# Optimization experiments

Measured on AMD Instinct MI355X. Metric: run time of the kernel, lower is better.

## Reference

```python
import jax, jax.numpy as jnp
import numpy as np

B, DIM, H, W = 4, 192, 256, 256
HEADS, DS = 6, 2
CPH = DIM // HEADS  # channels per head = 32
DN = ('NCHW', 'OIHW', 'NCHW')


def _conv(x, w, padding, groups=1):
    return jax.lax.conv_general_dilated(x, w, (1, 1), padding,
                                        dimension_numbers=DN,
                                        feature_group_count=groups)


def setup_inputs() -> dict:
    key = jax.random.key(0)
    ks = jax.random.split(key, 5)
    x = jax.random.normal(ks[0], (B, DIM, H, W), dtype=jnp.float32)
    temperature = jnp.ones((HEADS, 1, 1), dtype=jnp.float32)
    qkv_w = jax.random.normal(ks[1], (3 * DIM, DIM, 1, 1), dtype=jnp.float32) * 0.02
    dw_w = jax.random.normal(ks[2], (3 * DIM, 1, 3, 3), dtype=jnp.float32) * 0.02
    proj_w = jax.random.normal(ks[3], (DIM, DIM, 1, 1), dtype=jnp.float32) * 0.02
    a = jnp.full((1,), 0.2, dtype=jnp.float32)
    return {"x": x, "temperature": temperature, "qkv_w": qkv_w, "dw_w": dw_w,
            "proj_w": proj_w, "a1": a, "a2": a, "a3": a, "a4": a}


def _masked_softmax(attn, kk):
    # top-k mask per row (exact torch.topk + scatter_ semantics)
    _, idx = jax.lax.top_k(attn, kk)                      # [b,h,C,kk]
    mask = jax.nn.one_hot(idx, attn.shape[-1], dtype=jnp.bool_).any(axis=-2)
    return jax.nn.softmax(jnp.where(mask, attn, -jnp.inf), axis=-1)


def reference(x, temperature, qkv_w, dw_w, proj_w, a1, a2, a3, a4):
    b, c, h, w = x.shape
    h2, w2 = h // DS, w // DS
    # 1x1 qkv conv at full res, then exact adaptive (regular) max pool by DS
    qkv = _conv(x, qkv_w, 'VALID')                        # [b, 3*dim, h, w]
    qkv = jax.lax.reduce_window(qkv, -jnp.inf, jax.lax.max,
                                (1, 1, DS, DS), (1, 1, DS, DS), 'VALID')
    # depthwise 3x3
    qkv = _conv(qkv, dw_w, 'SAME', groups=3 * DIM)        # [b, 3*dim, h2, w2]
    q, k, v = jnp.split(qkv, 3, axis=1)
    n = h2 * w2
    q = q.reshape(b, HEADS, CPH, n)
    k = k.reshape(b, HEADS, CPH, n)
    v = v.reshape(b, HEADS, CPH, n)
    # F.normalize along last dim (eps clamp 1e-12)
    q = q / jnp.maximum(jnp.linalg.norm(q, axis=-1, keepdims=True), 1e-12)
    k = k / jnp.maximum(jnp.linalg.norm(k, axis=-1, keepdims=True), 1e-12)
    attn = jnp.einsum('bhcn,bhdn->bhcd', q, k) * temperature[None]  # [b,h,C,C]
    Cc = attn.shape[-1]
    att1 = _masked_softmax(attn, Cc // 2)
    att2 = _masked_softmax(attn, Cc * 2 // 3)
    att3 = _masked_softmax(attn, Cc * 3 // 4)
    att4 = _masked_softmax(attn, Cc * 4 // 5)
    def apply(a):
        return jnp.einsum('bhcd,bhdn->bhcn', a, v)
    out = apply(att1) * a1 + apply(att2) * a2 + apply(att3) * a3 + apply(att4) * a4
    out = out.reshape(b, DIM, h2, w2)
    out = jax.nn.gelu(out, approximate=False)
    # nearest upsample by integer factor DS
    out = jnp.repeat(jnp.repeat(out, DS, axis=2), DS, axis=3)
    out = _conv(out, proj_w, 'VALID')
    return out
```

## Files before the change

kernel.cpp:

```cpp
#include <hip/hip_runtime.h>
#include <hip/hip_bf16.h>
#include <math.h>

typedef __attribute__((ext_vector_type(8))) short bf16x8;
typedef __attribute__((ext_vector_type(4))) float f32x4;
typedef __attribute__((ext_vector_type(4))) unsigned int u32x4;

#define NP 16384
#define HWFULL 65536

__device__ __forceinline__ unsigned short f2bf(float f){
    union { float f; unsigned int u; } v; v.f = f;
    unsigned int u = v.u;
    u += 0x7fffu + ((u >> 16) & 1u);
    return (unsigned short)(u >> 16);
}
__device__ __forceinline__ float bf2f(unsigned short h){
    union { unsigned int u; float f; } v; v.u = ((unsigned int)h) << 16;
    return v.f;
}
__device__ __forceinline__ unsigned int pk2(float a, float b){
    return (unsigned int)f2bf(a) | ((unsigned int)f2bf(b) << 16);
}

__global__ void k_convert(const float* __restrict__ s, unsigned short* __restrict__ d, int n){
    int i = blockIdx.x * 256 + threadIdx.x;
    if (i < n) d[i] = f2bf(s[i]);
}

__global__ __launch_bounds__(256, 2)
void k_qkvpool(const float* __restrict__ x, const unsigned short* __restrict__ Wbf,
               unsigned short* __restrict__ qkvp){
    __shared__ unsigned short Bl[128*200];
    __shared__ unsigned short Ep[192*36];
    int tid = threadIdx.x;
    int lane = tid & 63, wv = tid >> 6;
    int n16 = lane & 15, quad = lane >> 4;
    int bx = blockIdx.x;
    int y2 = bx >> 2, x2blk = bx & 3;
    int b = blockIdx.y;

    #pragma unroll 6
    for (int j=0;j<12;j++){
        int idx = tid + j*256;
        int g = idx >> 7, w = idx & 127;
        int y = y2*2 + (w >> 6);
        int xc = x2blk*64 + (w & 63);
        const float* xp = x + (size_t)(b*192 + g*8) * HWFULL + y*256 + xc;
        float v0 = xp[0];
        float v1 = xp[(size_t)1*HWFULL];
        float v2 = xp[(size_t)2*HWFULL];
        float v3 = xp[(size_t)3*HWFULL];
        float v4 = xp[(size_t)4*HWFULL];
        float v5 = xp[(size_t)5*HWFULL];
        float v6 = xp[(size_t)6*HWFULL];
        float v7 = xp[(size_t)7*HWFULL];
        u32x4 pk;
        pk.x = pk2(v0,v1); pk.y = pk2(v2,v3); pk.z = pk2(v4,v5); pk.w = pk2(v6,v7);
        *(u32x4*)&Bl[w*200 + g*8] = pk;
    }
    bf16x8 afc[3], afn[3];
    #pragma unroll
    for (int j=0;j<3;j++)
        afc[j] = *(const bf16x8*)(Wbf + (size_t)(((wv*3+j)*16 + n16)*192 + quad*8));
    __syncthreads();

    for (int ocblk=0; ocblk<3; ocblk++){
        f32x4 acc[3][8];
        #pragma unroll
        for (int j=0;j<3;j++)
          #pragma unroll
          for (int s=0;s<8;s++)
            acc[j][s] = (f32x4){0.f,0.f,0.f,0.f};

        #pragma unroll 1
        for (int it=0; it<6; it++){
            int nocb = (it==5) ? ocblk+1 : ocblk;
            int nit  = (it==5) ? 0 : it+1;
            if (nocb < 3){
                #pragma unroll
                for (int j=0;j<3;j++)
                    afn[j] = *(const bf16x8*)(Wbf +
                        (size_t)((nocb*192 + (wv*3+j)*16 + n16)*192 + nit*32 + quad*8));
            }
            int bko = it*32 + quad*8;
            bf16x8 bfr[8];
            #pragma unroll
            for (int s=0;s<8;s++) bfr[s] = *(const bf16x8*)&Bl[(s*16 + n16)*200 + bko];
            #pragma unroll
            for (int j=0;j<3;j++)
              #pragma unroll
              for (int s=0;s<8;s++)
                acc[j][s] = __builtin_amdgcn_mfma_f32_16x16x32_bf16(afc[j], bfr[s], acc[j][s], 0,0,0);
            #pragma unroll
            for (int j=0;j<3;j++) afc[j] = afn[j];
        }
        __syncthreads();
        #pragma unroll
        for (int j=0;j<3;j++){
            int ocr = (wv*3+j)*16 + quad*4;
            #pragma unroll
            for (int sp=0;sp<4;sp++){
                #pragma unroll
                for (int r=0;r<4;r++){
                    float v = fmaxf(acc[j][sp][r], acc[j][sp+4][r]);
                    float o = __shfl_xor(v, 1, 64);
                    v = fmaxf(v, o);
                    if ((n16 & 1) == 0)
                        Ep[(ocr + r)*36 + sp*8 + (n16 >> 1)] = f2bf(v);
                }
            }
        }
        __syncthreads();
        size_t rowbase = (size_t)(b*576 + ocblk*192)*NP + y2*128 + x2blk*32;
        #pragma unroll
        for (int it=0; it<6; it++){
            int c = tid + it*256;
            int row = c >> 3, seg = c & 7;
            uint2 vv = *(const uint2*)&Ep[row*36 + seg*4];
            *(uint2*)(qkvp + rowbase + (size_t)row*NP + seg*4) = vv;
        }
    }
}

__global__ void k_dwconv(const unsigned short* __restrict__ qkvp, const float* __restrict__ dww,
                         float* __restrict__ dwout, float* __restrict__ sumsq){
    __shared__ float sl[18*130];
    int tid = threadIdx.x;
    int y0 = blockIdx.x * 16;
    int ch = blockIdx.y;
    int b  = blockIdx.z;
    const unsigned short* in = qkvp + (size_t)(b*576 + ch) * NP;
    #pragma unroll
    for (int j=0;j<10;j++){
        int idx = tid + j*256;
        if (idx < 18*130){
            int row = idx / 130;
            int col = idx % 130;
            int gy = y0 - 1 + row;
            int gx = col - 1;
            float v = 0.f;
            if (gy >= 0 && gy < 128 && gx >= 0 && gx < 128)
                v = bf2f(in[gy*128 + gx]);
            sl[idx] = v;
        }
    }
    float w0 = dww[ch*9+0], w1 = dww[ch*9+1], w2 = dww[ch*9+2];
    float w3 = dww[ch*9+3], w4 = dww[ch*9+4], w5 = dww[ch*9+5];
    float w6 = dww[ch*9+6], w7 = dww[ch*9+7], w8 = dww[ch*9+8];
    __syncthreads();
    float* outp = dwout + (size_t)(b*576 + ch) * NP;
    int col = tid & 127, half = tid >> 7;
    float ssq = 0.f;
    #pragma unroll
    for (int i=0;i<8;i++){
        int ry = half*8 + i;
        const float* r0 = &sl[ry*130 + col];
        float a = r0[0]*w0   + r0[1]*w1   + r0[2]*w2
                + r0[130]*w3 + r0[131]*w4 + r0[132]*w5
                + r0[260]*w6 + r0[261]*w7 + r0[262]*w8;
        outp[(y0+ry)*128 + col] = a;
        ssq += a*a;
    }
    if (ch < 384){
        #pragma unroll
        for (int off=32; off>0; off>>=1) ssq += __shfl_down(ssq, off, 64);
        if ((tid & 63) == 0) atomicAdd(&sumsq[b*384 + ch], ssq);
    }
}

__global__ __launch_bounds__(256) void k_attnraw(const float* __restrict__ dwout,
                                                 float* __restrict__ attn){
    __shared__ float sq[128*34];
    __shared__ float sk[128*34];
    int tid = threadIdx.x;
    int n0 = blockIdx.x * 512;
    int h = blockIdx.y, b = blockIdx.z;
    const float* qb = dwout + (size_t)(b*576 + h*32)*NP + n0;
    const float* kb = dwout + (size_t)(b*576 + 192 + h*32)*NP + n0;
    int s = tid >> 6, l = tid & 63;
    int c0 = (l & 7) * 4, d0 = (l >> 3) * 4;
    float acc[4][4];
    #pragma unroll
    for (int i=0;i<4;i++)
      #pragma unroll
      for (int j=0;j<4;j++) acc[i][j] = 0.f;

    for (int slc=0; slc<4; slc++){
        int nb = slc*128;
        __syncthreads();
        #pragma unroll 4
        for (int j=0;j<16;j++){
            int idx = tid + j*256;
            int r = idx >> 7, c = idx & 127;
            sq[c*34 + r] = qb[(size_t)r*NP + nb + c];
            sk[c*34 + r] = kb[(size_t)r*NP + nb + c];
        }
        __syncthreads();
        #pragma unroll 4
        for (int i=0;i<32;i++){
            int n = s*32 + i;
            const float* qp = &sq[n*34];
            const float* kp = &sk[n*34];
            float2 qa = *(const float2*)(qp + c0);
            float2 qc = *(const float2*)(qp + c0 + 2);
            float2 ka = *(const float2*)(kp + d0);
            float2 kc = *(const float2*)(kp + d0 + 2);
            float qv[4] = {qa.x, qa.y, qc.x, qc.y};
            float kv[4] = {ka.x, ka.y, kc.x, kc.y};
            #pragma unroll
            for (int ci=0;ci<4;ci++)
              #pragma unroll
              for (int di=0;di<4;di++)
                acc[ci][di] += qv[ci]*kv[di];
        }
    }
    __syncthreads();
    float* red = sq;
    #pragma unroll
    for (int ci=0;ci<4;ci++)
      #pragma unroll
      for (int di=0;di<4;di++)
        red[(s*32 + c0+ci)*33 + d0+di] = acc[ci][di];
    __syncthreads();
    float* ap = attn + (size_t)(b*6+h)*1024;
    #pragma unroll
    for (int j=0;j<4;j++){
        int o = tid + j*256;
        int c = o >> 5, d = o & 31;
        float v = red[(0*32 + c)*33 + d] + red[(1*32 + c)*33 + d]
                + red[(2*32 + c)*33 + d] + red[(3*32 + c)*33 + d];
        atomicAdd(ap + o, v);
    }
}

__global__ void k_mask_softmax(const float* __restrict__ attn, const float* __restrict__ sumsq,
                               const float* __restrict__ temp,
                               const float* __restrict__ A1, const float* __restrict__ A2,
                               const float* __restrict__ A3, const float* __restrict__ A4,
                               float* __restrict__ comb){
    __shared__ float Am[32][33];
    __shared__ float Em[32][33];
    __shared__ float qn[32], kn[32];
    __shared__ unsigned char Rm[32][32];
    int t = threadIdx.x;
    int bh = blockIdx.x;
    int b = bh / 6, h = bh % 6;
    if (t < 32){
        qn[t] = fmaxf(sqrtf(sumsq[b*384 + h*32 + t]), 1e-12f);
        kn[t] = fmaxf(sqrtf(sumsq[b*384 + 192 + h*32 + t]), 1e-12f);
    }
    __syncthreads();
    float tv = temp[h];
    const float* ap = attn + (size_t)bh*1024;
    #pragma unroll
    for (int j=0;j<16;j++){
        int idx = t + j*64;
        int c = idx >> 5, d = idx & 31;
        Am[c][d] = ap[idx] * tv / (qn[c]*kn[d]);
    }
    __syncthreads();
    if (t < 32){
        int c = t;
        float m = -1e30f;
        for (int d=0;d<32;d++) m = fmaxf(m, Am[c][d]);
        for (int d=0;d<32;d++) Em[c][d] = expf(Am[c][d] - m);
        for (int d=0;d<32;d++){
            float ad = Am[c][d];
            int rk = 0;
            for (int dd=0;dd<32;dd++){
                float av = Am[c][dd];
                rk += (av > ad) || (av == ad && dd < d);
            }
            Rm[c][d] = (unsigned char)rk;
        }
        float d0=0,d1=0,d2=0,d3=0;
        for (int d=0;d<32;d++){
            float e = Em[c][d]; int rk = Rm[c][d];
            if (rk < 16) d0 += e;
            if (rk < 21) d1 += e;
            if (rk < 24) d2 += e;
            if (rk < 25) d3 += e;
        }
        float f0 = A1[0]/d0, f1 = A2[0]/d1, f2 = A3[0]/d2, f3 = A4[0]/d3;
        float* cp = comb + (size_t)bh*1024 + c*32;
        for (int d=0;d<32;d++){
            int rk = Rm[c][d];
            float s = (rk<16?f0:0.f) + (rk<21?f1:0.f) + (rk<24?f2:0.f) + (rk<25?f3:0.f);
            cp[d] = Em[c][d] * s;
        }
    }
}

__global__ void k_applyv(const float* __restrict__ dwout, const float* __restrict__ comb,
                         unsigned short* __restrict__ gT){
    __shared__ float cm[3072];
    int tid = threadIdx.x;
    int b = blockIdx.y;
    int hz = blockIdx.z * 3;
    int n = blockIdx.x*256 + tid;
    #pragma unroll
    for (int j=0;j<12;j++) cm[tid + j*256] = comb[b*6144 + hz*1024 + tid + j*256];
    __syncthreads();
    const float* vb = dwout + (size_t)(b*576 + 384 + hz*32)*NP + n;
    unsigned short* gp = gT + (size_t)(b*NP + n)*192 + hz*32;
    #pragma unroll 1
    for (int h=0;h<3;h++){
        float v[32];
        #pragma unroll
        for (int d=0;d<32;d++) v[d] = vb[(size_t)(h*32+d)*NP];
        const float* chp = &cm[h*1024];
        #pragma unroll 1
        for (int cg=0;cg<4;cg++){
            float s[8];
            #pragma unroll
            for (int i=0;i<8;i++){
                const float* crow = chp + (cg*8+i)*32;
                float acc = 0.f;
                #pragma unroll
                for (int d=0;d<32;d++) acc += crow[d]*v[d];
                s[i] = 0.5f*acc*(1.f + erff(acc*0.70710678118654752f));
            }
            u32x4 pk;
            pk.x = pk2(s[0],s[1]); pk.y = pk2(s[2],s[3]);
            pk.z = pk2(s[4],s[5]); pk.w = pk2(s[6],s[7]);
            *(u32x4*)(gp + h*32 + cg*8) = pk;
        }
    }
}

__global__ __launch_bounds__(256, 2)
void k_proj(const unsigned short* __restrict__ gT, const unsigned short* __restrict__ Pbf,
            float* __restrict__ out){
    __shared__ unsigned short Bl[128*200];
    int tid = threadIdx.x;
    int lane = tid & 63, wv = tid >> 6;
    int n16 = lane & 15, quad = lane >> 4;
    int y2 = blockIdx.x, b = blockIdx.y;

    #pragma unroll 6
    for (int j=0;j<12;j++){
        int idx = tid + j*256;
        int r = idx / 24, g = idx - r*24;
        *(u32x4*)&Bl[r*200 + g*8] =
            *(const u32x4*)(gT + ((size_t)(b*NP + y2*128 + r)*192 + g*8));
    }
    bf16x8 afc[3], afn[3];
    #pragma unroll
    for (int j=0;j<3;j++)
        afc[j] = *(const bf16x8*)(Pbf + (size_t)(((wv*3+j)*16 + n16)*192 + quad*8));
    __syncthreads();

    f32x4 acc[3][8];
    #pragma unroll
    for (int j=0;j<3;j++)
      #pragma unroll
      for (int s=0;s<8;s++)
        acc[j][s] = (f32x4){0.f,0.f,0.f,0.f};

    #pragma unroll 1
    for (int it=0; it<6; it++){
        if (it < 5){
            #pragma unroll
            for (int j=0;j<3;j++)
                afn[j] = *(const bf16x8*)(Pbf +
                    (size_t)(((wv*3+j)*16 + n16)*192 + (it+1)*32 + quad*8));
        }
        int bko = it*32 + quad*8;
        bf16x8 bfr[8];
        #pragma unroll
        for (int s=0;s<8;s++) bfr[s] = *(const bf16x8*)&Bl[(s*16 + n16)*200 + bko];
        #pragma unroll
        for (int j=0;j<3;j++)
          #pragma unroll
          for (int s=0;s<8;s++)
            acc[j][s] = __builtin_amdgcn_mfma_f32_16x16x32_bf16(afc[j], bfr[s], acc[j][s], 0,0,0);
        #pragma unroll
        for (int j=0;j<3;j++) afc[j] = afn[j];
    }

    #pragma unroll
    for (int j=0;j<3;j++){
        int oc = (wv*3+j)*16 + quad*4;
        #pragma unroll
        for (int sp=0;sp<8;sp++){
            int x2 = sp*16 + n16;
            #pragma unroll
            for (int r=0;r<4;r++){
                float v = acc[j][sp][r];
                size_t o = ((size_t)(b*192 + oc + r)*256 + 2*y2)*256 + 2*x2;
                float2 val = make_float2(v, v);
                *(float2*)(out + o) = val;
                *(float2*)(out + o + 256) = val;
            }
        }
    }
}

extern "C" void kernel_launch(void* const* d_in, const int* in_sizes, int n_in,
                              void* d_out, int out_size, void* d_ws, size_t ws_size,
                              hipStream_t stream){
    const float* x     = (const float*)d_in[0];
    const float* temp  = (const float*)d_in[1];
    const float* qkvw  = (const float*)d_in[2];
    const float* dww   = (const float*)d_in[3];
    const float* projw = (const float*)d_in[4];
    const float* A1    = (const float*)d_in[5];
    const float* A2    = (const float*)d_in[6];
    const float* A3    = (const float*)d_in[7];
    const float* A4    = (const float*)d_in[8];
    float* out = (float*)d_out;
    char* ws = (char*)d_ws;

    float*          dwout = (float*)ws;
    unsigned short* qkvp  = (unsigned short*)(ws + 150994944ull);
    unsigned short* gT    = (unsigned short*)(ws + 150994944ull);
    unsigned short* Wbf   = (unsigned short*)(ws + 226492416ull);
    unsigned short* Pbf   = (unsigned short*)(ws + 226713600ull);
    float*          attn  = (float*)(ws + 226787328ull);
    float*          comb  = (float*)(ws + 226885632ull);
    float*          sumsq = (float*)(ws + 226983936ull);

    hipMemsetAsync(attn, 0, 98304, stream);
    hipMemsetAsync(sumsq, 0, 6144, stream);
    k_convert<<<dim3((110592+255)/256), dim3(256), 0, stream>>>(qkvw, Wbf, 110592);
    k_convert<<<dim3((36864+255)/256), dim3(256), 0, stream>>>(projw, Pbf, 36864);
    k_qkvpool<<<dim3(512,4), dim3(256), 0, stream>>>(x, Wbf, qkvp);
    k_dwconv<<<dim3(8,576,4), dim3(256), 0, stream>>>(qkvp, dww, dwout, sumsq);
    k_attnraw<<<dim3(32,6,4), dim3(256), 0, stream>>>(dwout, attn);
    k_mask_softmax<<<dim3(24), dim3(64), 0, stream>>>(attn, sumsq, temp, A1, A2, A3, A4, comb);
    k_applyv<<<dim3(64,4,2), dim3(256), 0, stream>>>(dwout, comb, gT);
    k_proj<<<dim3(128,4), dim3(256), 0, stream>>>(gT, Pbf, out);
}
```

Measured before the change: 643.9 us.

## Halve qkvpool tile for higher occupancy and vectorize dwconv halo loads

The qkv 1x1-conv+maxpool kernel now processes 64 pixels per block instead of 128, halving LDS and accumulator registers so four blocks per CU can be resident, with twice as many blocks launched. The weight-fragment prefetch across iterations is dropped in favour of plain per-iteration loads. The depthwise conv loads its input rows as packed bf16 pairs with a padded LDS stride and sets the zero borders explicitly. It also slides a 3-row register window to avoid reloading rows from LDS. Smaller tiles mean each weight fragment is reused across fewer pixels, so weight traffic goes up.

```diff
diff --git a/kernel.cpp b/kernel.cpp
--- a/kernel.cpp
+++ b/kernel.cpp
@@ -28,24 +28,24 @@
     if (i < n) d[i] = f2bf(s[i]);
 }
 
-__global__ __launch_bounds__(256, 2)
+__global__ __launch_bounds__(256, 4)
 void k_qkvpool(const float* __restrict__ x, const unsigned short* __restrict__ Wbf,
                unsigned short* __restrict__ qkvp){
-    __shared__ unsigned short Bl[128*200];
-    __shared__ unsigned short Ep[192*36];
+    __shared__ unsigned short Bl[64*200];
+    __shared__ unsigned short Ep[192*20];
     int tid = threadIdx.x;
     int lane = tid & 63, wv = tid >> 6;
     int n16 = lane & 15, quad = lane >> 4;
     int bx = blockIdx.x;
-    int y2 = bx >> 2, x2blk = bx & 3;
+    int y2 = bx >> 3, x2blk = bx & 7;
     int b = blockIdx.y;
 
-    #pragma unroll 6
-    for (int j=0;j<12;j++){
+    #pragma unroll 3
+    for (int j=0;j<6;j++){
         int idx = tid + j*256;
-        int g = idx >> 7, w = idx & 127;
-        int y = y2*2 + (w >> 6);
-        int xc = x2blk*64 + (w & 63);
+        int g = idx >> 6, w = idx & 63;
+        int y = y2*2 + (w >> 5);
+        int xc = x2blk*32 + (w & 31);
         const float* xp = x + (size_t)(b*192 + g*8) * HWFULL + y*256 + xc;
         float v0 = xp[0];
         float v1 = xp[(size_t)1*HWFULL];
@@ -59,65 +59,56 @@
         pk.x = pk2(v0,v1); pk.y = pk2(v2,v3); pk.z = pk2(v4,v5); pk.w = pk2(v6,v7);
         *(u32x4*)&Bl[w*200 + g*8] = pk;
     }
-    bf16x8 afc[3], afn[3];
-    #pragma unroll
-    for (int j=0;j<3;j++)
-        afc[j] = *(const bf16x8*)(Wbf + (size_t)(((wv*3+j)*16 + n16)*192 + quad*8));
     __syncthreads();
 
     for (int ocblk=0; ocblk<3; ocblk++){
-        f32x4 acc[3][8];
+        f32x4 acc[3][4];
         #pragma unroll
         for (int j=0;j<3;j++)
           #pragma unroll
-          for (int s=0;s<8;s++)
+          for (int s=0;s<4;s++)
             acc[j][s] = (f32x4){0.f,0.f,0.f,0.f};
 
         #pragma unroll 1
         for (int it=0; it<6; it++){
-            int nocb = (it==5) ? ocblk+1 : ocblk;
-            int nit  = (it==5) ? 0 : it+1;
-            if (nocb < 3){
-                #pragma unroll
-                for (int j=0;j<3;j++)
-                    afn[j] = *(const bf16x8*)(Wbf +
-                        (size_t)((nocb*192 + (wv*3+j)*16 + n16)*192 + nit*32 + quad*8));
-            }
+            bf16x8 af[3];
+            #pragma unroll
+            for (int j=0;j<3;j++)
+                af[j] = *(const bf16x8*)(Wbf +
+                    (size_t)((ocblk*192 + (wv*3+j)*16 + n16)*192 + it*32 + quad*8));
             int bko = it*32 + quad*8;
-            bf16x8 bfr[8];
-            #pragma unroll
-            for (int s=0;s<8;s++) bfr[s] = *(const bf16x8*)&Bl[(s*16 + n16)*200 + bko];
+            bf16x8 bfr[4];
+            #pragma unroll
+            for (int s=0;s<4;s++) bfr[s] = *(const bf16x8*)&Bl[(s*16 + n16)*200 + bko];
             #pragma unroll
             for (int j=0;j<3;j++)
               #pragma unroll
-              for (int s=0;s<8;s++)
-                acc[j][s] = __builtin_amdgcn_mfma_f32_16x16x32_bf16(afc[j], bfr[s], acc[j][s], 0,0,0);
-            #pragma unroll
-            for (int j=0;j<3;j++) afc[j] = afn[j];
+              for (int s=0;s<4;s++)
+                acc[j][s] = __builtin_amdgcn_mfma_f32_16x16x32_bf16(af[j], bfr[s], acc[j][s], 0,0,0);
         }
         __syncthreads();
         #pragma unroll
         for (int j=0;j<3;j++){
             int ocr = (wv*3+j)*16 + quad*4;
             #pragma unroll
-            for (int sp=0;sp<4;sp++){
+            for (int sp=0;sp<2;sp++){
                 #pragma unroll
                 for (int r=0;r<4;r++){
-                    float v = fmaxf(acc[j][sp][r], acc[j][sp+4][r]);
+                    float v = fmaxf(acc[j][sp][r], acc[j][sp+2][r]);
                     float o = __shfl_xor(v, 1, 64);
                     v = fmaxf(v, o);
                     if ((n16 & 1) == 0)
-                        Ep[(ocr + r)*36 + sp*8 + (n16 >> 1)] = f2bf(v);
+                        Ep[(ocr + r)*20 + sp*8 + (n16 >> 1)] = f2bf(v);
                 }
             }
         }
         __syncthreads();
-        size_t rowbase = (size_t)(b*576 + ocblk*192)*NP + y2*128 + x2blk*32;
-        #pragma unroll
-        for (int it=0; it<6; it++){
-            int c = tid + it*256;
-            int row = c >> 3, seg = c & 7;
-            uint2 vv = *(const uint2*)&Ep[row*36 + seg*4];
+        size_t rowbase = (size_t)(b*576 + ocblk*192)*NP + y2*128 + x2blk*16;
+        #pragma unroll
+        for (int it2=0; it2<3; it2++){
+            int c = tid + it2*256;
+            int row = c >> 2, seg = c & 3;
+            uint2 vv = *(const uint2*)&Ep[row*20 + seg*4];
             *(uint2*)(qkvp + rowbase + (size_t)row*NP + seg*4) = vv;
         }
     }
@@ -125,26 +116,29 @@
 
 __global__ void k_dwconv(const unsigned short* __restrict__ qkvp, const float* __restrict__ dww,
                          float* __restrict__ dwout, float* __restrict__ sumsq){
-    __shared__ float sl[18*130];
+    __shared__ float sl[18*132];
     int tid = threadIdx.x;
     int y0 = blockIdx.x * 16;
     int ch = blockIdx.y;
     int b  = blockIdx.z;
     const unsigned short* in = qkvp + (size_t)(b*576 + ch) * NP;
-    #pragma unroll
-    for (int j=0;j<10;j++){
-        int idx = tid + j*256;
-        if (idx < 18*130){
-            int row = idx / 130;
-            int col = idx % 130;
+    int l = tid & 63, wr = tid >> 6;
+    #pragma unroll
+    for (int j=0;j<5;j++){
+        int row = wr + j*4;
+        if (row < 18){
             int gy = y0 - 1 + row;
-            int gx = col - 1;
-            float v = 0.f;
-            if (gy >= 0 && gy < 128 && gx >= 0 && gx < 128)
-                v = bf2f(in[gy*128 + gx]);
-            sl[idx] = v;
-        }
-    }
+            float2 v = make_float2(0.f, 0.f);
+            if (gy >= 0 && gy < 128){
+                unsigned int u = *(const unsigned int*)&in[gy*128 + l*2];
+                v.x = bf2f((unsigned short)(u & 0xffffu));
+                v.y = bf2f((unsigned short)(u >> 16));
+            }
+            *(float2*)&sl[row*132 + 2 + l*2] = v;
+        }
+    }
+    if (tid < 18) sl[tid*132 + 1] = 0.f;
+    else if (tid < 36) sl[(tid-18)*132 + 130] = 0.f;
     float w0 = dww[ch*9+0], w1 = dww[ch*9+1], w2 = dww[ch*9+2];
     float w3 = dww[ch*9+3], w4 = dww[ch*9+4], w5 = dww[ch*9+5];
     float w6 = dww[ch*9+6], w7 = dww[ch*9+7], w8 = dww[ch*9+8];
@@ -152,15 +146,20 @@
     float* outp = dwout + (size_t)(b*576 + ch) * NP;
     int col = tid & 127, half = tid >> 7;
     float ssq = 0.f;
+    int base = (half*8)*132 + col + 1;
+    float r0a=sl[base],     r0b=sl[base+1],   r0c=sl[base+2];
+    float r1a=sl[base+132], r1b=sl[base+133], r1c=sl[base+134];
     #pragma unroll
     for (int i=0;i<8;i++){
-        int ry = half*8 + i;
-        const float* r0 = &sl[ry*130 + col];
-        float a = r0[0]*w0   + r0[1]*w1   + r0[2]*w2
-                + r0[130]*w3 + r0[131]*w4 + r0[132]*w5
-                + r0[260]*w6 + r0[261]*w7 + r0[262]*w8;
-        outp[(y0+ry)*128 + col] = a;
+        const float* r2 = &sl[base + (i+2)*132];
+        float r2a=r2[0], r2b=r2[1], r2c=r2[2];
+        float a = r0a*w0 + r0b*w1 + r0c*w2
+                + r1a*w3 + r1b*w4 + r1c*w5
+                + r2a*w6 + r2b*w7 + r2c*w8;
+        outp[(y0 + half*8 + i)*128 + col] = a;
         ssq += a*a;
+        r0a=r1a; r0b=r1b; r0c=r1c;
+        r1a=r2a; r1b=r2b; r1c=r2c;
     }
     if (ch < 384){
         #pragma unroll
@@ -425,7 +424,7 @@
     hipMemsetAsync(sumsq, 0, 6144, stream);
     k_convert<<<dim3((110592+255)/256), dim3(256), 0, stream>>>(qkvw, Wbf, 110592);
     k_convert<<<dim3((36864+255)/256), dim3(256), 0, stream>>>(projw, Pbf, 36864);
-    k_qkvpool<<<dim3(512,4), dim3(256), 0, stream>>>(x, Wbf, qkvp);
+    k_qkvpool<<<dim3(1024,4), dim3(256), 0, stream>>>(x, Wbf, qkvp);
     k_dwconv<<<dim3(8,576,4), dim3(256), 0, stream>>>(qkvp, dww, dwout, sumsq);
     k_attnraw<<<dim3(32,6,4), dim3(256), 0, stream>>>(dwout, attn);
     k_mask_softmax<<<dim3(24), dim3(64), 0, stream>>>(attn, sumsq, temp, A1, A2, A3, A4, comb);
```

After: 658.7 us. 2.3% more time.

## Pre-transpose input to pixel-major bf16 and vectorize depthwise conv loads

Applied to the files above, without the earlier changes.

Adds a separate kernel that converts x to bf16 in a pixel-major layout grouped by 2x2 pool windows, so the qkv/pool GEMM kernel loads its B tile with contiguous 16-byte reads instead of strided scalar fp32 loads. The max-pool epilogue is reworked to reduce across four adjacent lanes to match the new pixel ordering. Separately, the depthwise conv now stages each row with vectorized loads into padded shared memory and reuses rows across output rows through registers. The change adds one extra round trip of the input through HBM (about 50MB of bf16 written and read) in exchange for coalesced access.

```diff
diff --git a/kernel.cpp b/kernel.cpp
--- a/kernel.cpp
+++ b/kernel.cpp
@@ -28,8 +28,39 @@
     if (i < n) d[i] = f2bf(s[i]);
 }
 
+__global__ __launch_bounds__(256) void k_xpose(const float* __restrict__ x,
+                                               unsigned short* __restrict__ xT){
+    int tid = threadIdx.x;
+    int y2 = blockIdx.x, b = blockIdx.y;
+    size_t pbase = (size_t)b*65536 + (size_t)y2*512;
+    #pragma unroll 1
+    for (int it=0; it<6; it++){
+        int idx = tid + it*256;
+        int g = idx >> 6, xq = idx & 63;
+        const float* xp = x + ((size_t)(b*192 + g*8))*HWFULL + (size_t)(y2*2)*256 + xq*4;
+        f32x4 rv[16];
+        #pragma unroll
+        for (int j=0;j<8;j++){
+            rv[j]   = *(const f32x4*)(xp + (size_t)j*HWFULL);
+            rv[8+j] = *(const f32x4*)(xp + (size_t)j*HWFULL + 256);
+        }
+        #pragma unroll
+        for (int r=0;r<2;r++){
+            #pragma unroll
+            for (int xi=0; xi<4; xi++){
+                u32x4 pk;
+                pk.x = pk2(rv[r*8+0][xi], rv[r*8+1][xi]);
+                pk.y = pk2(rv[r*8+2][xi], rv[r*8+3][xi]);
+                pk.z = pk2(rv[r*8+4][xi], rv[r*8+5][xi]);
+                pk.w = pk2(rv[r*8+6][xi], rv[r*8+7][xi]);
+                *(u32x4*)(xT + (pbase + (size_t)(xq*4+xi)*2 + r)*192 + g*8) = pk;
+            }
+        }
+    }
+}
+
 __global__ __launch_bounds__(256, 2)
-void k_qkvpool(const float* __restrict__ x, const unsigned short* __restrict__ Wbf,
+void k_qkvpool(const unsigned short* __restrict__ xT, const unsigned short* __restrict__ Wbf,
                unsigned short* __restrict__ qkvp){
     __shared__ unsigned short Bl[128*200];
     __shared__ unsigned short Ep[192*36];
@@ -40,24 +71,12 @@
     int y2 = bx >> 2, x2blk = bx & 3;
     int b = blockIdx.y;
 
+    const unsigned short* src = xT + ((size_t)b*65536 + (size_t)y2*512 + x2blk*128)*192;
     #pragma unroll 6
     for (int j=0;j<12;j++){
         int idx = tid + j*256;
-        int g = idx >> 7, w = idx & 127;
-        int y = y2*2 + (w >> 6);
-        int xc = x2blk*64 + (w & 63);
-        const float* xp = x + (size_t)(b*192 + g*8) * HWFULL + y*256 + xc;
-        float v0 = xp[0];
-        float v1 = xp[(size_t)1*HWFULL];
-        float v2 = xp[(size_t)2*HWFULL];
-        float v3 = xp[(size_t)3*HWFULL];
-        float v4 = xp[(size_t)4*HWFULL];
-        float v5 = xp[(size_t)5*HWFULL];
-        float v6 = xp[(size_t)6*HWFULL];
-        float v7 = xp[(size_t)7*HWFULL];
-        u32x4 pk;
-        pk.x = pk2(v0,v1); pk.y = pk2(v2,v3); pk.z = pk2(v4,v5); pk.w = pk2(v6,v7);
-        *(u32x4*)&Bl[w*200 + g*8] = pk;
+        int r = idx / 24, g = idx - r*24;
+        *(u32x4*)&Bl[r*200 + g*8] = *(const u32x4*)(src + (size_t)r*192 + g*8);
     }
     bf16x8 afc[3], afn[3];
     #pragma unroll
@@ -100,22 +119,22 @@
         for (int j=0;j<3;j++){
             int ocr = (wv*3+j)*16 + quad*4;
             #pragma unroll
-            for (int sp=0;sp<4;sp++){
+            for (int s=0;s<8;s++){
                 #pragma unroll
                 for (int r=0;r<4;r++){
-                    float v = fmaxf(acc[j][sp][r], acc[j][sp+4][r]);
-                    float o = __shfl_xor(v, 1, 64);
-                    v = fmaxf(v, o);
-                    if ((n16 & 1) == 0)
-                        Ep[(ocr + r)*36 + sp*8 + (n16 >> 1)] = f2bf(v);
+                    float v = acc[j][s][r];
+                    v = fmaxf(v, __shfl_xor(v, 1, 64));
+                    v = fmaxf(v, __shfl_xor(v, 2, 64));
+                    if ((n16 & 3) == 0)
+                        Ep[(ocr + r)*36 + s*4 + (n16 >> 2)] = f2bf(v);
                 }
             }
         }
         __syncthreads();
         size_t rowbase = (size_t)(b*576 + ocblk*192)*NP + y2*128 + x2blk*32;
         #pragma unroll
-        for (int it=0; it<6; it++){
-            int c = tid + it*256;
+        for (int it2=0; it2<6; it2++){
+            int c = tid + it2*256;
             int row = c >> 3, seg = c & 7;
             uint2 vv = *(const uint2*)&Ep[row*36 + seg*4];
             *(uint2*)(qkvp + rowbase + (size_t)row*NP + seg*4) = vv;
@@ -125,26 +144,29 @@
 
 __global__ void k_dwconv(const unsigned short* __restrict__ qkvp, const float* __restrict__ dww,
                          float* __restrict__ dwout, float* __restrict__ sumsq){
-    __shared__ float sl[18*130];
+    __shared__ float sl[18*132];
     int tid = threadIdx.x;
     int y0 = blockIdx.x * 16;
     int ch = blockIdx.y;
     int b  = blockIdx.z;
     const unsigned short* in = qkvp + (size_t)(b*576 + ch) * NP;
-    #pragma unroll
-    for (int j=0;j<10;j++){
-        int idx = tid + j*256;
-        if (idx < 18*130){
-            int row = idx / 130;
-            int col = idx % 130;
+    int l = tid & 63, wr = tid >> 6;
+    #pragma unroll
+    for (int j=0;j<5;j++){
+        int row = wr + j*4;
+        if (row < 18){
             int gy = y0 - 1 + row;
-            int gx = col - 1;
-            float v = 0.f;
-            if (gy >= 0 && gy < 128 && gx >= 0 && gx < 128)
-                v = bf2f(in[gy*128 + gx]);
-            sl[idx] = v;
-        }
-    }
+            float2 v = make_float2(0.f, 0.f);
+            if (gy >= 0 && gy < 128){
+                unsigned int u = *(const unsigned int*)&in[gy*128 + l*2];
+                v.x = bf2f((unsigned short)(u & 0xffffu));
+                v.y = bf2f((unsigned short)(u >> 16));
+            }
+            *(float2*)&sl[row*132 + 2 + l*2] = v;
+        }
+    }
+    if (tid < 18) sl[tid*132 + 1] = 0.f;
+    else if (tid < 36) sl[(tid-18)*132 + 130] = 0.f;
     float w0 = dww[ch*9+0], w1 = dww[ch*9+1], w2 = dww[ch*9+2];
     float w3 = dww[ch*9+3], w4 = dww[ch*9+4], w5 = dww[ch*9+5];
     float w6 = dww[ch*9+6], w7 = dww[ch*9+7], w8 = dww[ch*9+8];
@@ -152,15 +174,20 @@
     float* outp = dwout + (size_t)(b*576 + ch) * NP;
     int col = tid & 127, half = tid >> 7;
     float ssq = 0.f;
+    int base = (half*8)*132 + col + 1;
+    float r0a=sl[base],     r0b=sl[base+1],   r0c=sl[base+2];
+    float r1a=sl[base+132], r1b=sl[base+133], r1c=sl[base+134];
     #pragma unroll
     for (int i=0;i<8;i++){
-        int ry = half*8 + i;
-        const float* r0 = &sl[ry*130 + col];
-        float a = r0[0]*w0   + r0[1]*w1   + r0[2]*w2
-                + r0[130]*w3 + r0[131]*w4 + r0[132]*w5
-                + r0[260]*w6 + r0[261]*w7 + r0[262]*w8;
-        outp[(y0+ry)*128 + col] = a;
+        const float* r2 = &sl[base + (i+2)*132];
+        float r2a=r2[0], r2b=r2[1], r2c=r2[2];
+        float a = r0a*w0 + r0b*w1 + r0c*w2
+                + r1a*w3 + r1b*w4 + r1c*w5
+                + r2a*w6 + r2b*w7 + r2c*w8;
+        outp[(y0 + half*8 + i)*128 + col] = a;
         ssq += a*a;
+        r0a=r1a; r0b=r1b; r0c=r1c;
+        r1a=r2a; r1b=r2b; r1c=r2c;
     }
     if (ch < 384){
         #pragma unroll
@@ -413,6 +440,7 @@
     char* ws = (char*)d_ws;
 
     float*          dwout = (float*)ws;
+    unsigned short* xT    = (unsigned short*)ws;
     unsigned short* qkvp  = (unsigned short*)(ws + 150994944ull);
     unsigned short* gT    = (unsigned short*)(ws + 150994944ull);
     unsigned short* Wbf   = (unsigned short*)(ws + 226492416ull);
@@ -425,7 +453,8 @@
     hipMemsetAsync(sumsq, 0, 6144, stream);
     k_convert<<<dim3((110592+255)/256), dim3(256), 0, stream>>>(qkvw, Wbf, 110592);
     k_convert<<<dim3((36864+255)/256), dim3(256), 0, stream>>>(projw, Pbf, 36864);
-    k_qkvpool<<<dim3(512,4), dim3(256), 0, stream>>>(x, Wbf, qkvp);
+    k_xpose<<<dim3(128,4), dim3(256), 0, stream>>>(x, xT);
+    k_qkvpool<<<dim3(512,4), dim3(256), 0, stream>>>(xT, Wbf, qkvp);
     k_dwconv<<<dim3(8,576,4), dim3(256), 0, stream>>>(qkvp, dww, dwout, sumsq);
     k_attnraw<<<dim3(32,6,4), dim3(256), 0, stream>>>(dwout, attn);
     k_mask_softmax<<<dim3(24), dim3(64), 0, stream>>>(attn, sumsq, temp, A1, A2, A3, A4, comb);
```

Result: slower. 765.6 us (+18.9%).
